# Kernel tuning notes

Measured on AMD Instinct MI355X. Metric: run time of the kernel, lower is better.

The kernel has to match this reference:

```python
import jax, jax.numpy as jnp
import numpy as np

IN, HID, NCLS = 16, 50, 20


def setup_inputs() -> dict:
    key = jax.random.key(0)
    ks = jax.random.split(key, 7)
    B, T = 8192, 128
    s_ih = 1.0 / np.sqrt(HID)
    return {
        "x": jax.random.normal(ks[0], (B, T, IN), dtype=jnp.float32),
        # PyTorch LSTM params, gate order (i, f, g, o)
        "W_ih": jax.random.uniform(ks[1], (4 * HID, IN), jnp.float32, -s_ih, s_ih),
        "W_hh": jax.random.uniform(ks[2], (4 * HID, HID), jnp.float32, -s_ih, s_ih),
        "b_ih": jax.random.uniform(ks[3], (4 * HID,), jnp.float32, -s_ih, s_ih),
        "b_hh": jax.random.uniform(ks[4], (4 * HID,), jnp.float32, -s_ih, s_ih),
        "W_fc": jax.random.uniform(ks[5], (NCLS, HID), jnp.float32, -s_ih, s_ih),
        "b_fc": jax.random.uniform(ks[6], (NCLS,), jnp.float32, -s_ih, s_ih),
    }


def _lstm_last_hidden(x, W_ih, W_hh, b_ih, b_hh):
    # x: [B, T, IN] -> precompute input projections for all steps: [T, B, 4H]
    B = x.shape[0]
    xg = jnp.einsum("bti,gi->tbg", x, W_ih) + (b_ih + b_hh)

    def step(carry, xg_t):
        h, c = carry
        gates = xg_t + h @ W_hh.T  # [B, 4H]
        i, f, g, o = jnp.split(gates, 4, axis=-1)
        i = jax.nn.sigmoid(i)
        f = jax.nn.sigmoid(f)
        g = jnp.tanh(g)
        o = jax.nn.sigmoid(o)
        c = f * c + i * g
        h = o * jnp.tanh(c)
        return (h, c), None

    h0 = jnp.zeros((B, HID), x.dtype)
    c0 = jnp.zeros((B, HID), x.dtype)
    (hT, _), _ = jax.lax.scan(step, (h0, c0), xg)
    return hT  # == out[:, -1, :]


def reference(x, W_ih, W_hh, b_ih, b_hh, W_fc, b_fc):
    hT = _lstm_last_hidden(x.astype(jnp.float32), W_ih, W_hh, b_ih, b_hh)
    # dropout is identity in eval mode; relu then linear head on last timestep
    feat = jax.nn.relu(hT)
    logits = feat @ W_fc.T + b_fc  # [B, NCLS]
    return logits
```

## Files before the change

kernel.cpp:

```cpp
#include <hip/hip_runtime.h>

#define IN_    16
#define HID_   50
#define T_     128
#define NCLS_  20
#define BPB_   16
#define NTHR_  512
#define KP_    96
#define KPW_   48

typedef _Float16 half8 __attribute__((ext_vector_type(8)));
typedef float    f32x4 __attribute__((ext_vector_type(4)));
typedef unsigned int u32;

#define L2E_ 1.4426950408889634f
__device__ __forceinline__ u32 pkh2(float a, float b) {
    union { u32 v; _Float16 h[2]; } p; p.h[0] = (_Float16)a; p.h[1] = (_Float16)b; return p.v;
}
#define MFMA(A, B, C) __builtin_amdgcn_mfma_f32_16x16x32_f16((A), (B), (C), 0, 0, 0)
#define SIGS(v)  __builtin_amdgcn_rcpf(1.0f + __builtin_amdgcn_exp2f(v))
#define TANHS(v) fmaf(2.0f, __builtin_amdgcn_rcpf(1.0f + __builtin_amdgcn_exp2f(v)), -1.0f)

__device__ __forceinline__ half8 load_afrag(const float* __restrict__ W_ih,
                                            const float* __restrict__ W_hh,
                                            const float* __restrict__ b_ih,
                                            const float* __restrict__ b_hh,
                                            int s, int c, int q) {
    half8 r = {};
    const int u = s >> 2, kk = s & 3;
    if (u < HID_) {
        const float sc = (kk == 2) ? (-2.0f * L2E_) : (-L2E_);
        const int g = kk * HID_ + u;
        #pragma unroll
        for (int e = 0; e < 8; ++e) {
            const int k = c * 32 + q * 8 + e;
            float w = 0.f;
            if (k < IN_)                 w = W_ih[g * IN_ + k];
            else if (k < IN_ + HID_)     w = W_hh[g * HID_ + (k - IN_)];
            else if (k == IN_ + HID_)    w = b_ih[g] + b_hh[g];
            r[e] = (_Float16)(w * sc);
        }
    }
    return r;
}

__global__ __launch_bounds__(NTHR_, 4)
void lstm_mfma(const float* __restrict__ x,
               const float* __restrict__ W_ih,
               const float* __restrict__ W_hh,
               const float* __restrict__ b_ih,
               const float* __restrict__ b_hh,
               const float* __restrict__ W_fc,
               const float* __restrict__ b_fc,
               float* __restrict__ out)
{
    __shared__ __align__(16) _Float16 st[2][BPB_ * KP_];

    const int tid  = threadIdx.x;
    const int lane = tid & 63;
    const int wv   = tid >> 6;
    const int b0   = blockIdx.x * BPB_;
    const bool comp = (wv < 7);

    for (int idx = tid; idx < 2 * BPB_ * KPW_; idx += NTHR_)
        ((u32*)st)[idx] = ((idx % KPW_) == 33) ? 0x00003C00u : 0u;

    const int q  = lane >> 4;
    const int s0 = 2 * wv * 16 + (lane & 15);
    const int s1 = s0 + 16;
    half8 A00 = {}, A01 = {}, A02 = {}, A10 = {}, A11 = {}, A12 = {};
    if (comp) {
        A00 = load_afrag(W_ih, W_hh, b_ih, b_hh, s0, 0, q);
        A01 = load_afrag(W_ih, W_hh, b_ih, b_hh, s0, 1, q);
        A02 = load_afrag(W_ih, W_hh, b_ih, b_hh, s0, 2, q);
        A10 = load_afrag(W_ih, W_hh, b_ih, b_hh, s1, 0, q);
        A11 = load_afrag(W_ih, W_hh, b_ih, b_hh, s1, 1, q);
        A12 = load_afrag(W_ih, W_hh, b_ih, b_hh, s1, 2, q);
    }

    const int u0 = 8 * wv + q;
    const int u1 = u0 + 4;
    float c0_ = 0.f, c1_ = 0.f;

    const int bcol  = lane & 15;
    const int brow  = bcol * KP_ + q * 8;
    const int hrow0 = bcol * KP_ + IN_ + u0;
    const int hrow1 = bcol * KP_ + IN_ + u1;

    const int lb = lane >> 2, fq = lane & 3;
    const float* xq = x + (size_t)(b0 + lb) * (T_ * IN_) + 4 * fq;
    const int xo = lb * KPW_ + 2 * fq;

    float4 xr = {0.f, 0.f, 0.f, 0.f};
    __syncthreads();
    if (!comp) {
        const float4 v = *(const float4*)xq;
        u32* d = (u32*)st[0];
        d[xo] = pkh2(v.x, v.y); d[xo + 1] = pkh2(v.z, v.w);
        xr = *(const float4*)(xq + IN_);
    }
    __syncthreads();

    for (int t = 0; t < T_; ++t) {
        const _Float16* sc = st[t & 1];
        _Float16*       sn = st[(t & 1) ^ 1];

        if (comp) {
            const half8 B0 = *(const half8*)(sc + brow);
            const half8 B1 = *(const half8*)(sc + brow + 32);
            const half8 B2 = *(const half8*)(sc + brow + 64);
            const f32x4 Z = {0.f, 0.f, 0.f, 0.f};
            f32x4 C0 = MFMA(A00, B0, Z);
            f32x4 C1 = MFMA(A10, B0, Z);
            C0 = MFMA(A01, B1, C0);
            C1 = MFMA(A11, B1, C1);
            C0 = MFMA(A02, B2, C0);
            C1 = MFMA(A12, B2, C1);

            {
                const float iv = SIGS(C0[0]), fv = SIGS(C0[1]);
                const float gv = TANHS(C0[2]), ov = SIGS(C0[3]);
                c0_ = fmaf(fv, c0_, iv * gv);
                const float hv = ov * TANHS(c0_ * (-2.0f * L2E_));
                if (u0 < HID_) sn[hrow0] = (_Float16)hv;
            }
            {
                const float iv = SIGS(C1[0]), fv = SIGS(C1[1]);
                const float gv = TANHS(C1[2]), ov = SIGS(C1[3]);
                c1_ = fmaf(fv, c1_, iv * gv);
                const float hv = ov * TANHS(c1_ * (-2.0f * L2E_));
                if (u1 < HID_) sn[hrow1] = (_Float16)hv;
            }
        } else {
            if (t + 1 < T_) {
                u32* d = (u32*)sn;
                d[xo] = pkh2(xr.x, xr.y); d[xo + 1] = pkh2(xr.z, xr.w);
            }
            if (t + 2 < T_) xr = *(const float4*)(xq + (size_t)(t + 2) * IN_);
        }
        __syncthreads();
    }

    const _Float16* hf = st[0];

    if (tid < BPB_ * NCLS_) {
        const int b  = tid / NCLS_;
        const int cl = tid - b * NCLS_;
        float acc = b_fc[cl];
        #pragma unroll
        for (int j = 0; j < HID_; ++j) {
            const float hv = fmaxf((float)hf[b * KP_ + IN_ + j], 0.0f);
            acc = fmaf(hv, W_fc[cl * HID_ + j], acc);
        }
        out[(size_t)(b0 + b) * NCLS_ + cl] = acc;
    }
}

extern "C" void kernel_launch(void* const* d_in, const int* in_sizes, int n_in,
                              void* d_out, int out_size, void* d_ws, size_t ws_size,
                              hipStream_t stream) {
    const float* x    = (const float*)d_in[0];
    const float* W_ih = (const float*)d_in[1];
    const float* W_hh = (const float*)d_in[2];
    const float* b_ih = (const float*)d_in[3];
    const float* b_hh = (const float*)d_in[4];
    const float* W_fc = (const float*)d_in[5];
    const float* b_fc = (const float*)d_in[6];
    float* out = (float*)d_out;

    const int B = in_sizes[0] / (T_ * IN_);
    dim3 grid(B / BPB_), block(NTHR_);
    hipLaunchKernelGGL(lstm_mfma, grid, block, 0, stream,
                       x, W_ih, W_hh, b_ih, b_hh, W_fc, b_fc, out);
}
```

Before: 99.00 us.

## Split gate rows across 13 compute waves, one MFMA tile per wave

Raises the block to 14 waves so 13 compute waves each own one 16-row tile of the gate matrix instead of 7 waves owning two tiles each. This halves the serial MFMA chain and activation work per wave on every timestep, which shortens the per-step critical path of the recurrence. The LDS row stride is also padded from 96 to 104 halves, likely to reduce bank conflicts. In exchange it costs more waves per block, more barrier participants per step, and fewer resident blocks per CU.

Result: slower. 128.6 us (+29.9%).

```diff
diff --git a/kernel.cpp b/kernel.cpp
--- a/kernel.cpp
+++ b/kernel.cpp
@@ -5,9 +5,9 @@
 #define T_     128
 #define NCLS_  20
 #define BPB_   16
-#define NTHR_  512
-#define KP_    96
-#define KPW_   48
+#define NTHR_  896
+#define KP_    104
+#define KPW_   52
 
 typedef _Float16 half8 __attribute__((ext_vector_type(8)));
 typedef float    f32x4 __attribute__((ext_vector_type(4)));
@@ -44,7 +44,7 @@
     return r;
 }
 
-__global__ __launch_bounds__(NTHR_, 4)
+__global__ __launch_bounds__(NTHR_, 7)
 void lstm_mfma(const float* __restrict__ x,
                const float* __restrict__ W_ih,
                const float* __restrict__ W_hh,
@@ -60,32 +60,26 @@
     const int lane = tid & 63;
     const int wv   = tid >> 6;
     const int b0   = blockIdx.x * BPB_;
-    const bool comp = (wv < 7);
+    const bool comp = (wv < 13);
 
     for (int idx = tid; idx < 2 * BPB_ * KPW_; idx += NTHR_)
         ((u32*)st)[idx] = ((idx % KPW_) == 33) ? 0x00003C00u : 0u;
 
-    const int q  = lane >> 4;
-    const int s0 = 2 * wv * 16 + (lane & 15);
-    const int s1 = s0 + 16;
-    half8 A00 = {}, A01 = {}, A02 = {}, A10 = {}, A11 = {}, A12 = {};
+    const int q = lane >> 4;
+    const int s = wv * 16 + (lane & 15);
+    half8 A0 = {}, A1 = {}, A2 = {};
     if (comp) {
-        A00 = load_afrag(W_ih, W_hh, b_ih, b_hh, s0, 0, q);
-        A01 = load_afrag(W_ih, W_hh, b_ih, b_hh, s0, 1, q);
-        A02 = load_afrag(W_ih, W_hh, b_ih, b_hh, s0, 2, q);
-        A10 = load_afrag(W_ih, W_hh, b_ih, b_hh, s1, 0, q);
-        A11 = load_afrag(W_ih, W_hh, b_ih, b_hh, s1, 1, q);
-        A12 = load_afrag(W_ih, W_hh, b_ih, b_hh, s1, 2, q);
+        A0 = load_afrag(W_ih, W_hh, b_ih, b_hh, s, 0, q);
+        A1 = load_afrag(W_ih, W_hh, b_ih, b_hh, s, 1, q);
+        A2 = load_afrag(W_ih, W_hh, b_ih, b_hh, s, 2, q);
     }
 
-    const int u0 = 8 * wv + q;
-    const int u1 = u0 + 4;
-    float c0_ = 0.f, c1_ = 0.f;
+    const int u = 4 * wv + q;
+    float c_ = 0.f;
 
-    const int bcol  = lane & 15;
-    const int brow  = bcol * KP_ + q * 8;
-    const int hrow0 = bcol * KP_ + IN_ + u0;
-    const int hrow1 = bcol * KP_ + IN_ + u1;
+    const int bcol = lane & 15;
+    const int brow = bcol * KP_ + q * 8;
+    const int hrow = bcol * KP_ + IN_ + u;
 
     const int lb = lane >> 2, fq = lane & 3;
     const float* xq = x + (size_t)(b0 + lb) * (T_ * IN_) + 4 * fq;
@@ -110,27 +104,15 @@
             const half8 B1 = *(const half8*)(sc + brow + 32);
             const half8 B2 = *(const half8*)(sc + brow + 64);
             const f32x4 Z = {0.f, 0.f, 0.f, 0.f};
-            f32x4 C0 = MFMA(A00, B0, Z);
-            f32x4 C1 = MFMA(A10, B0, Z);
-            C0 = MFMA(A01, B1, C0);
-            C1 = MFMA(A11, B1, C1);
-            C0 = MFMA(A02, B2, C0);
-            C1 = MFMA(A12, B2, C1);
+            f32x4 C = MFMA(A0, B0, Z);
+            C = MFMA(A1, B1, C);
+            C = MFMA(A2, B2, C);
 
-            {
-                const float iv = SIGS(C0[0]), fv = SIGS(C0[1]);
-                const float gv = TANHS(C0[2]), ov = SIGS(C0[3]);
-                c0_ = fmaf(fv, c0_, iv * gv);
-                const float hv = ov * TANHS(c0_ * (-2.0f * L2E_));
-                if (u0 < HID_) sn[hrow0] = (_Float16)hv;
-            }
-            {
-                const float iv = SIGS(C1[0]), fv = SIGS(C1[1]);
-                const float gv = TANHS(C1[2]), ov = SIGS(C1[3]);
-                c1_ = fmaf(fv, c1_, iv * gv);
-                const float hv = ov * TANHS(c1_ * (-2.0f * L2E_));
-                if (u1 < HID_) sn[hrow1] = (_Float16)hv;
-            }
+            const float iv = SIGS(C[0]), fv = SIGS(C[1]);
+            const float gv = TANHS(C[2]), ov = SIGS(C[3]);
+            c_ = fmaf(fv, c_, iv * gv);
+            const float hv = ov * TANHS(c_ * (-2.0f * L2E_));
+            if (u < HID_) sn[hrow] = (_Float16)hv;
         } else {
             if (t + 1 < T_) {
                 u32* d = (u32*)sn;
```
